# Kernel optimization log

Hardware: AMD Instinct MI355X
Metric: run time of the kernel (lower is better)

## Reference

```python
import jax, jax.numpy as jnp
import numpy as np

INPUT_DIM = 1024
NUM_HEADS = 16
HEAD_DIM = INPUT_DIM // NUM_HEADS


def setup_inputs() -> dict:
    key = jax.random.key(0)
    ks = jax.random.split(key, 9)
    d = INPUT_DIM
    s = 1.0 / np.sqrt(d)
    x = jax.random.normal(ks[0], (2, 2048, d), dtype=jnp.float32)
    # nn.Linear default init ~ U(-1/sqrt(in), 1/sqrt(in)); weights stored as (out, in), we keep (in, out)
    Wq = jax.random.uniform(ks[1], (d, d), jnp.float32, -s, s)
    bq = jax.random.uniform(ks[2], (d,), jnp.float32, -s, s)
    Wk = jax.random.uniform(ks[3], (d, d), jnp.float32, -s, s)
    bk = jax.random.uniform(ks[4], (d,), jnp.float32, -s, s)
    Wv = jax.random.uniform(ks[5], (d, d), jnp.float32, -s, s)
    bv = jax.random.uniform(ks[6], (d,), jnp.float32, -s, s)
    Wo = jax.random.uniform(ks[7], (d, d), jnp.float32, -s, s)
    bo = jax.random.uniform(ks[8], (d,), jnp.float32, -s, s)
    return {"x": x, "Wq": Wq, "bq": bq, "Wk": Wk, "bk": bk, "Wv": Wv, "bv": bv, "Wo": Wo, "bo": bo}


def reference(x, Wq, bq, Wk, bk, Wv, bv, Wo, bo):
    b, t, d = x.shape
    h, hd = NUM_HEADS, HEAD_DIM
    # projections -> [b, h, t, hd]
    q = (x @ Wq + bq).reshape(b, t, h, hd).transpose(0, 2, 1, 3)
    k = (x @ Wk + bk).reshape(b, t, h, hd).transpose(0, 2, 1, 3)
    v = (x @ Wv + bv).reshape(b, t, h, hd).transpose(0, 2, 1, 3)
    scores = jnp.einsum('bhqd,bhkd->bhqk', q, k) / jnp.sqrt(jnp.float32(hd))
    probs = jax.nn.softmax(scores, axis=-1)
    out = jnp.einsum('bhqk,bhkd->bhqd', probs, v)
    out = out.transpose(0, 2, 1, 3).reshape(b, t, d)
    return out @ Wo + bo
```

## Files before the change

### kernel.cpp

```cpp
#include <hip/hip_runtime.h>
#include <math.h>


#define BATCH 2
#define SEQ   2048
#define DIM   1024
#define NHEAD 16
#define HDIM  64
#define MROWS (BATCH * SEQ)
#define BH    (BATCH * NHEAD)
#define NKT   (SEQ / 64)

typedef __attribute__((ext_vector_type(4))) float     floatx4;
typedef __attribute__((ext_vector_type(4))) float     float4v;
typedef __attribute__((ext_vector_type(8))) _Float16  half8;
typedef __attribute__((ext_vector_type(4))) _Float16  half4;
typedef __attribute__((ext_vector_type(2))) __fp16    fp16x2;
typedef __attribute__((ext_vector_type(4))) unsigned  uint4v;

#define SOFT_C 5.77078016f
#define QSCALE 0.18033688f

#if __has_builtin(__builtin_amdgcn_exp2f)
#define EXP2F(x) __builtin_amdgcn_exp2f(x)
#else
#define EXP2F(x) exp2f(x)
#endif

__device__ __forceinline__ void gload16(const void* g, void* l) {
    __builtin_amdgcn_global_load_lds(
        (const __attribute__((address_space(1))) unsigned int*)g,
        (__attribute__((address_space(3))) unsigned int*)l, 16, 0, 0);
}

__device__ __forceinline__ unsigned pk2(float a, float b) {
    fp16x2 v = __builtin_amdgcn_cvt_pkrtz(a, b);
    return __builtin_bit_cast(unsigned, v);
}

__device__ __forceinline__ void plswap(unsigned &a, unsigned &b) {
#if __has_builtin(__builtin_amdgcn_permlane32_swap) && __has_builtin(__builtin_amdgcn_permlane16_swap)
    auto r32 = __builtin_amdgcn_permlane32_swap(a, b, false, false);
    auto r16 = __builtin_amdgcn_permlane16_swap(r32[0], r32[1], false, false);
    a = r16[0]; b = r16[1];
#else
    asm volatile("s_nop 1\n\t"
                 "v_permlane32_swap_b32 %0, %1\n\t"
                 "s_nop 1\n\t"
                 "v_permlane16_swap_b32 %0, %1\n\t"
                 "s_nop 1"
                 : "+v"(a), "+v"(b));
#endif
}

__global__ __launch_bounds__(256) void prep(
    const float* __restrict__ x,
    const float* __restrict__ Wq, const float* __restrict__ Wk,
    const float* __restrict__ Wv, const float* __restrict__ Wo,
    _Float16* __restrict__ xh,
    _Float16* __restrict__ Wqt, _Float16* __restrict__ Wkt,
    _Float16* __restrict__ Wvt, _Float16* __restrict__ Wot)
{
    const int tid = threadIdx.x;
    if (blockIdx.z == 4) {
        const int bid = blockIdx.y * 16 + blockIdx.x;
        #pragma unroll
        for (int it = 0; it < 8; ++it) {
            const size_t i = (((size_t)it * 256 + bid) * 256 + tid) * 8;
            float4v a = *(const float4v*)(x + i);
            float4v b = *(const float4v*)(x + i + 4);
            half8 o;
            #pragma unroll
            for (int c = 0; c < 4; ++c) { o[c] = (_Float16)a[c]; o[4+c] = (_Float16)b[c]; }
            *(half8*)(xh + i) = o;
        }
        return;
    }
    __shared__ float tile[64][65];
    const float* W; _Float16* o;
    switch (blockIdx.z) {
        case 0: W = Wq; o = Wqt; break;
        case 1: W = Wk; o = Wkt; break;
        case 2: W = Wv; o = Wvt; break;
        default: W = Wo; o = Wot; break;
    }
    const int n0 = blockIdx.x * 64, k0 = blockIdx.y * 64;
    #pragma unroll
    for (int p = 0; p < 16; ++p) {
        int idx = tid + p * 256;
        int r = idx >> 6, c = idx & 63;
        tile[r][c] = W[(size_t)(k0 + r) * DIM + n0 + c];
    }
    __syncthreads();
    #pragma unroll
    for (int p = 0; p < 16; ++p) {
        int idx = tid + p * 256;
        int r = idx >> 6, c = idx & 63;
        o[(size_t)(n0 + r) * DIM + k0 + c] = (_Float16)tile[c][r];
    }
}

__device__ __forceinline__ void gemm_core16(
    const _Float16* __restrict__ Ap, const _Float16* __restrict__ Bp,
    int m0, int n0, _Float16* AL, _Float16* BL, floatx4 acc[4][4])
{
    const int tid  = threadIdx.x;
    const int wave = tid >> 6;
    const int lane = tid & 63;
    const int li   = lane & 15;
    const int quad = lane >> 4;
    const int wm   = (wave >> 1) * 64;
    const int wn   = (wave & 1) * 64;

    for (int kt = 0; kt < DIM / 64; ++kt) {
        __syncthreads();
        const int k0 = kt * 64;
        #pragma unroll
        for (int p = 0; p < 4; ++p) {
            int s = tid + p * 256;
            int r = s >> 3, ks = s & 7;
            int kg = (ks ^ (r & 7)) << 3;
            int ldsb = (wave * 64 + p * 256) * 8;
            gload16(Ap + (size_t)(m0 + r) * DIM + k0 + kg, AL + ldsb);
            gload16(Bp + (size_t)(n0 + r) * DIM + k0 + kg, BL + ldsb);
        }
        __syncthreads();

        half8 a[4][2], b[4][2];
        #pragma unroll
        for (int i = 0; i < 4; ++i) {
            int ra = (wm + i * 16 + li) << 6;
            int rb = (wn + i * 16 + li) << 6;
            #pragma unroll
            for (int h = 0; h < 2; ++h) {
                a[i][h] = *(const half8*)(AL + ra + (((h * 4 + quad) ^ (li & 7)) << 3));
                b[i][h] = *(const half8*)(BL + rb + (((h * 4 + quad) ^ (li & 7)) << 3));
            }
        }
        #pragma unroll
        for (int i = 0; i < 4; ++i)
            #pragma unroll
            for (int j = 0; j < 4; ++j) {
                acc[i][j] = __builtin_amdgcn_mfma_f32_16x16x32_f16(a[i][0], b[j][0], acc[i][j], 0, 0, 0);
                acc[i][j] = __builtin_amdgcn_mfma_f32_16x16x32_f16(a[i][1], b[j][1], acc[i][j], 0, 0, 0);
            }
    }
}

__global__ __launch_bounds__(256, 2) void qkv_mfma(
    const _Float16* __restrict__ xh,
    const _Float16* __restrict__ Wqt, const _Float16* __restrict__ Wkt,
    const _Float16* __restrict__ Wvt,
    const float* __restrict__ bq, const float* __restrict__ bk,
    const float* __restrict__ bv,
    _Float16* __restrict__ Qh, _Float16* __restrict__ Kh,
    _Float16* __restrict__ Vth)
{
    __shared__ __align__(16) _Float16 SH[128 * 128];
    _Float16* AL = SH;
    _Float16* BL = SH + 128 * 64;

    const int bid = blockIdx.x + 8 * (blockIdx.y + 32 * blockIdx.z);
    const int swz = (bid & 7) * 96 + (bid >> 3);
    const int bx  = swz & 7;
    const int by  = (swz >> 3) & 31;
    const int z   = swz >> 8;

    const _Float16* Bp; const float* bias;
    if (z == 0)      { Bp = Wqt; bias = bq; }
    else if (z == 1) { Bp = Wkt; bias = bk; }
    else             { Bp = Wvt; bias = bv; }

    const int m0 = by * 128, n0 = bx * 128;

    floatx4 acc[4][4];
    #pragma unroll
    for (int i = 0; i < 4; ++i)
        #pragma unroll
        for (int j = 0; j < 4; ++j) acc[i][j] = (floatx4){0.f, 0.f, 0.f, 0.f};

    gemm_core16(xh, Bp, m0, n0, AL, BL, acc);

    const int tid = threadIdx.x, wave = tid >> 6, lane = tid & 63;
    const int li = lane & 15, quad = lane >> 4;
    const int wm = (wave >> 1) * 64, wn = (wave & 1) * 64;
    const int bb = m0 >> 11, t0 = m0 & 2047;

    if (z != 2) {
        _Float16* out = (z == 0) ? Qh : Kh;
        const float sc = (z == 0) ? QSCALE : 1.0f;
        #pragma unroll
        for (int i = 0; i < 4; ++i)
            #pragma unroll
            for (int j = 0; j < 4; ++j) {
                int n = n0 + wn + j * 16 + li;
                int h = n >> 6, hd = n & 63;
                float b_ = bias[n];
                #pragma unroll
                for (int r = 0; r < 4; ++r) {
                    int m = m0 + wm + i * 16 + quad * 4 + r;
                    int t = m & 2047;
                    out[(((size_t)(bb * NHEAD + h) * SEQ) + t) * HDIM + hd] =
                        (_Float16)((acc[i][j][r] + b_) * sc);
                }
            }
    } else {
        __syncthreads();
        #pragma unroll
        for (int i = 0; i < 4; ++i)
            #pragma unroll
            for (int j = 0; j < 4; ++j) {
                int n = wn + j * 16 + li;
                float b_ = bias[n0 + n];
                half4 w;
                #pragma unroll
                for (int r = 0; r < 4; ++r) w[r] = (_Float16)(acc[i][j][r] + b_);
                int col  = wm + i * 16 + quad * 4;
                int colp = ((((col >> 3) ^ (n & 7)) << 3)) | (col & 7);
                *(half4*)(SH + n * 128 + colp) = w;
            }
        __syncthreads();
        #pragma unroll
        for (int p = 0; p < 8; ++p) {
            int idx = p * 256 + tid;
            int v = idx >> 4, c8 = (idx & 15) * 8;
            int c8p = (((c8 >> 3) ^ (v & 7)) << 3);
            half8 w = *(const half8*)(SH + v * 128 + c8p);
            int n = n0 + v;
            int h = n >> 6, hd = n & 63;
            *(half8*)(Vth + ((size_t)(bb * NHEAD + h) * HDIM + hd) * SEQ + t0 + c8) = w;
        }
    }
}

__global__ __launch_bounds__(256, 4) void attn(
    const _Float16* __restrict__ Q, const _Float16* __restrict__ K,
    const _Float16* __restrict__ Vt,
    _Float16* __restrict__ Ctx)
{
    __shared__ __align__(16) _Float16 Ks[2][64 * 64];
    __shared__ __align__(16) _Float16 Vs[2][64 * 64];

    const int tid  = threadIdx.x;
    const int wave = tid >> 6;
    const int lane = tid & 63;
    const int li   = lane & 15;
    const int quad = lane >> 4;

    const int bid = blockIdx.x + 16 * blockIdx.y;
    const int swz = (bid & 7) * 64 + (bid >> 3);
    const int q0  = (swz & 15) * 128;
    const int bh  = swz >> 4;
    const int b   = bh >> 4, h = bh & 15;

    half8 qa[2][2];
    #pragma unroll
    for (int nq = 0; nq < 2; ++nq) {
        size_t qrow = ((size_t)bh * SEQ + q0 + wave * 32 + nq * 16 + li) * HDIM;
        qa[nq][0] = *(const half8*)(Q + qrow + quad * 8);
        qa[nq][1] = *(const half8*)(Q + qrow + 32 + quad * 8);
    }

    half8 onesA;
    {
        _Float16 v = (li == 0) ? (_Float16)1.0f : (_Float16)0.0f;
        #pragma unroll
        for (int c = 0; c < 8; ++c) onesA[c] = v;
    }

    floatx4 O[4][2];
    floatx4 rsacc[2];
    #pragma unroll
    for (int nq = 0; nq < 2; ++nq) {
        rsacc[nq] = (floatx4){0.f, 0.f, 0.f, 0.f};
        #pragma unroll
        for (int i = 0; i < 4; ++i) O[i][nq] = (floatx4){0.f, 0.f, 0.f, 0.f};
    }

    const _Float16* Kbh = K  + (size_t)bh * SEQ * HDIM;
    const _Float16* Vbh = Vt + (size_t)bh * HDIM * SEQ;

    auto stage = [&](int buf, int kt_) {
        const _Float16* Kg = Kbh + (size_t)kt_ * 64 * HDIM;
        const _Float16* Vg = Vbh + kt_ * 64;
        _Float16* Kl = &Ks[buf][0];
        _Float16* Vl = &Vs[buf][0];
        #pragma unroll
        for (int p = 0; p < 2; ++p) {
            int s = tid + p * 256;
            int r = s >> 3, ks = s & 7;
            int kg = (ks ^ (r & 7)) << 3;
            int ldsb = (wave * 64 + p * 256) * 8;
            gload16(Kg + r * HDIM + kg, Kl + ldsb);
            gload16(Vg + (size_t)r * SEQ + kg, Vl + ldsb);
        }
    };

    stage(0, 0);
    __syncthreads();
    int cur = 0;

    for (int kt = 0; kt < NKT; ++kt) {
        if (kt + 1 < NKT) stage(cur ^ 1, kt + 1);
        const _Float16* Kc = &Ks[cur][0];
        const _Float16* Vc = &Vs[cur][0];

        __builtin_amdgcn_s_setprio(1);

        unsigned R[2][4][2];
        #pragma unroll
        for (int mb = 0; mb < 4; ++mb) {
            int row = (mb * 16 + li) << 6;
            half8 a0 = *(const half8*)(Kc + row + ((quad ^ (li & 7)) << 3));
            half8 a1 = *(const half8*)(Kc + row + (((quad + 4) ^ (li & 7)) << 3));
            #pragma unroll
            for (int nq = 0; nq < 2; ++nq) {
                floatx4 st = (floatx4){-SOFT_C, -SOFT_C, -SOFT_C, -SOFT_C};
                st = __builtin_amdgcn_mfma_f32_16x16x32_f16(a0, qa[nq][0], st, 0, 0, 0);
                st = __builtin_amdgcn_mfma_f32_16x16x32_f16(a1, qa[nq][1], st, 0, 0, 0);
                R[nq][mb][0] = pk2(EXP2F(st[0]), EXP2F(st[1]));
                R[nq][mb][1] = pk2(EXP2F(st[2]), EXP2F(st[3]));
            }
        }

        half8 pb[2][2];
        #pragma unroll
        for (int nq = 0; nq < 2; ++nq)
            #pragma unroll
            for (int f = 0; f < 2; ++f) {
                unsigned w0, w1, w2, w3;
                {
                    unsigned x = R[nq][2 * f][0], y = R[nq][2 * f + 1][0];
                    plswap(x, y);
                    w0 = x; w2 = y;
                }
                {
                    unsigned x = R[nq][2 * f][1], y = R[nq][2 * f + 1][1];
                    plswap(x, y);
                    w1 = x; w3 = y;
                }
                uint4v uw; uw[0] = w0; uw[1] = w1; uw[2] = w2; uw[3] = w3;
                pb[nq][f] = __builtin_bit_cast(half8, uw);
            }

        #pragma unroll
        for (int nq = 0; nq < 2; ++nq) {
            rsacc[nq] = __builtin_amdgcn_mfma_f32_16x16x32_f16(onesA, pb[nq][0], rsacc[nq], 0, 0, 0);
            rsacc[nq] = __builtin_amdgcn_mfma_f32_16x16x32_f16(onesA, pb[nq][1], rsacc[nq], 0, 0, 0);
        }
        #pragma unroll
        for (int mb = 0; mb < 4; ++mb) {
            int row = (mb * 16 + li) << 6;
            half8 v0 = *(const half8*)(Vc + row + ((quad ^ (li & 7)) << 3));
            half8 v1 = *(const half8*)(Vc + row + (((quad + 4) ^ (li & 7)) << 3));
            #pragma unroll
            for (int nq = 0; nq < 2; ++nq) {
                O[mb][nq] = __builtin_amdgcn_mfma_f32_16x16x32_f16(v0, pb[nq][0], O[mb][nq], 0, 0, 0);
                O[mb][nq] = __builtin_amdgcn_mfma_f32_16x16x32_f16(v1, pb[nq][1], O[mb][nq], 0, 0, 0);
            }
        }

        __builtin_amdgcn_s_setprio(0);

        __syncthreads();
        cur ^= 1;
    }

    float inv[2];
    #pragma unroll
    for (int nq = 0; nq < 2; ++nq) {
        float rs = __shfl(rsacc[nq][0], li, 64);
        inv[nq] = 1.0f / rs;
    }

    _Float16* Sw = &Ks[0][0] + wave * (32 * 64);
    #pragma unroll
    for (int mb = 0; mb < 4; ++mb)
        #pragma unroll
        for (int nq = 0; nq < 2; ++nq) {
            uint2 w;
            w.x = pk2(O[mb][nq][0] * inv[nq], O[mb][nq][1] * inv[nq]);
            w.y = pk2(O[mb][nq][2] * inv[nq], O[mb][nq][3] * inv[nq]);
            int row = nq * 16 + li;
            int col = mb * 16 + quad * 4;
            int swc = (((col >> 3) ^ (row & 7)) << 3) | (col & 7);
            *(uint2*)(Sw + row * 64 + swc) = w;
        }
    __builtin_amdgcn_s_waitcnt(0);
    #pragma unroll
    for (int p = 0; p < 4; ++p) {
        int idx = p * 64 + lane;
        int qq = idx >> 3, c = idx & 7;
        half8 v = *(const half8*)(Sw + qq * 64 + ((c ^ (qq & 7)) << 3));
        size_t row = (size_t)b * SEQ + q0 + wave * 32 + qq;
        *(half8*)(Ctx + row * DIM + h * HDIM + c * 8) = v;
    }
}

__global__ __launch_bounds__(256, 2) void out_mfma(
    const _Float16* __restrict__ Ctx, const _Float16* __restrict__ Wot,
    const float* __restrict__ bo, float* __restrict__ out)
{
    __shared__ __align__(16) _Float16 AL[128 * 64];
    __shared__ __align__(16) _Float16 BL[128 * 64];

    const int bid = blockIdx.x + 8 * blockIdx.y;
    const int swz = (bid & 7) * 32 + (bid >> 3);
    const int m0 = (swz >> 3) * 128, n0 = (swz & 7) * 128;

    floatx4 acc[4][4];
    #pragma unroll
    for (int i = 0; i < 4; ++i)
        #pragma unroll
        for (int j = 0; j < 4; ++j) acc[i][j] = (floatx4){0.f, 0.f, 0.f, 0.f};

    gemm_core16(Ctx, Wot, m0, n0, AL, BL, acc);

    const int tid = threadIdx.x, wave = tid >> 6, lane = tid & 63;
    const int li = lane & 15, quad = lane >> 4;
    const int wm = (wave >> 1) * 64, wn = (wave & 1) * 64;

    #pragma unroll
    for (int i = 0; i < 4; ++i)
        #pragma unroll
        for (int j = 0; j < 4; ++j) {
            int n = n0 + wn + j * 16 + li;
            float b_ = bo[n];
            #pragma unroll
            for (int r = 0; r < 4; ++r) {
                int m = m0 + wm + i * 16 + quad * 4 + r;
                out[(size_t)m * DIM + n] = acc[i][j][r] + b_;
            }
        }
}

extern "C" void kernel_launch(void* const* d_in, const int* in_sizes, int n_in,
                              void* d_out, int out_size, void* d_ws, size_t ws_size,
                              hipStream_t stream) {
    const float* x  = (const float*)d_in[0];
    const float* Wq = (const float*)d_in[1];
    const float* bq = (const float*)d_in[2];
    const float* Wk = (const float*)d_in[3];
    const float* bk = (const float*)d_in[4];
    const float* Wv = (const float*)d_in[5];
    const float* bv = (const float*)d_in[6];
    const float* Wo = (const float*)d_in[7];
    const float* bo = (const float*)d_in[8];
    float* out = (float*)d_out;

    const size_t PX = (size_t)MROWS * DIM;
    const size_t PW = (size_t)DIM * DIM;
    _Float16* xh  = (_Float16*)d_ws;
    _Float16* Wqt = xh + PX;
    _Float16* Wkt = Wqt + PW;
    _Float16* Wvt = Wkt + PW;
    _Float16* Wot = Wvt + PW;
    _Float16* Qh  = Wot + PW;
    _Float16* Kh  = Qh + PX;
    _Float16* spare = Kh + PX;
    _Float16* Vth = spare + PX;

    _Float16* Ctx = xh;

    prep<<<dim3(16, 16, 5), 256, 0, stream>>>(
        x, Wq, Wk, Wv, Wo, xh, Wqt, Wkt, Wvt, Wot);

    qkv_mfma<<<dim3(DIM / 128, MROWS / 128, 3), 256, 0, stream>>>(
        xh, Wqt, Wkt, Wvt, bq, bk, bv, Qh, Kh, Vth);

    attn<<<dim3(SEQ / 128, BH), 256, 0, stream>>>(
        Qh, Kh, Vth, Ctx);

    out_mfma<<<dim3(DIM / 128, MROWS / 128), 256, 0, stream>>>(
        Ctx, Wot, bo, out);
}
```

Measured before the change: 179.7 us.

## Split attention head dimension of V across two blocks to double grid size

```diff
diff --git a/kernel.cpp b/kernel.cpp
--- a/kernel.cpp
+++ b/kernel.cpp
@@ -239,7 +239,7 @@
     _Float16* __restrict__ Ctx)
 {
     __shared__ __align__(16) _Float16 Ks[2][64 * 64];
-    __shared__ __align__(16) _Float16 Vs[2][64 * 64];
+    __shared__ __align__(16) _Float16 Vs[2][32 * 64];
 
     const int tid  = threadIdx.x;
     const int wave = tid >> 6;
@@ -247,11 +247,13 @@
     const int li   = lane & 15;
     const int quad = lane >> 4;
 
-    const int bid = blockIdx.x + 16 * blockIdx.y;
-    const int swz = (bid & 7) * 64 + (bid >> 3);
+    const int bid = blockIdx.x + 16 * (blockIdx.y + 2 * blockIdx.z);
+    const int swz = (bid & 7) * 128 + (bid >> 3);
     const int q0  = (swz & 15) * 128;
-    const int bh  = swz >> 4;
+    const int hh  = (swz >> 4) & 1;
+    const int bh  = swz >> 5;
     const int b   = bh >> 4, h = bh & 15;
+    const int hd0 = hh * 32;
 
     half8 qa[2][2];
     #pragma unroll
@@ -268,17 +270,17 @@
         for (int c = 0; c < 8; ++c) onesA[c] = v;
     }
 
-    floatx4 O[4][2];
+    floatx4 O[2][2];
     floatx4 rsacc[2];
     #pragma unroll
     for (int nq = 0; nq < 2; ++nq) {
         rsacc[nq] = (floatx4){0.f, 0.f, 0.f, 0.f};
         #pragma unroll
-        for (int i = 0; i < 4; ++i) O[i][nq] = (floatx4){0.f, 0.f, 0.f, 0.f};
+        for (int i = 0; i < 2; ++i) O[i][nq] = (floatx4){0.f, 0.f, 0.f, 0.f};
     }
 
     const _Float16* Kbh = K  + (size_t)bh * SEQ * HDIM;
-    const _Float16* Vbh = Vt + (size_t)bh * HDIM * SEQ;
+    const _Float16* Vbh = Vt + ((size_t)bh * HDIM + hd0) * SEQ;
 
     auto stage = [&](int buf, int kt_) {
         const _Float16* Kg = Kbh + (size_t)kt_ * 64 * HDIM;
@@ -290,9 +292,12 @@
             int s = tid + p * 256;
             int r = s >> 3, ks = s & 7;
             int kg = (ks ^ (r & 7)) << 3;
-            int ldsb = (wave * 64 + p * 256) * 8;
-            gload16(Kg + r * HDIM + kg, Kl + ldsb);
-            gload16(Vg + (size_t)r * SEQ + kg, Vl + ldsb);
+            gload16(Kg + r * HDIM + kg, Kl + (wave * 64 + p * 256) * 8);
+        }
+        {
+            int r = tid >> 3, ks = tid & 7;
+            int kg = (ks ^ (r & 7)) << 3;
+            gload16(Vg + (size_t)r * SEQ + kg, Vl + wave * 64 * 8);
         }
     };
 
@@ -349,14 +354,14 @@
             rsacc[nq] = __builtin_amdgcn_mfma_f32_16x16x32_f16(onesA, pb[nq][1], rsacc[nq], 0, 0, 0);
         }
         #pragma unroll
-        for (int mb = 0; mb < 4; ++mb) {
-            int row = (mb * 16 + li) << 6;
+        for (int vb = 0; vb < 2; ++vb) {
+            int row = (vb * 16 + li) << 6;
             half8 v0 = *(const half8*)(Vc + row + ((quad ^ (li & 7)) << 3));
             half8 v1 = *(const half8*)(Vc + row + (((quad + 4) ^ (li & 7)) << 3));
             #pragma unroll
             for (int nq = 0; nq < 2; ++nq) {
-                O[mb][nq] = __builtin_amdgcn_mfma_f32_16x16x32_f16(v0, pb[nq][0], O[mb][nq], 0, 0, 0);
-                O[mb][nq] = __builtin_amdgcn_mfma_f32_16x16x32_f16(v1, pb[nq][1], O[mb][nq], 0, 0, 0);
+                O[vb][nq] = __builtin_amdgcn_mfma_f32_16x16x32_f16(v0, pb[nq][0], O[vb][nq], 0, 0, 0);
+                O[vb][nq] = __builtin_amdgcn_mfma_f32_16x16x32_f16(v1, pb[nq][1], O[vb][nq], 0, 0, 0);
             }
         }
 
@@ -373,27 +378,27 @@
         inv[nq] = 1.0f / rs;
     }
 
-    _Float16* Sw = &Ks[0][0] + wave * (32 * 64);
-    #pragma unroll
-    for (int mb = 0; mb < 4; ++mb)
+    _Float16* Sw = &Ks[0][0] + wave * (32 * 32);
+    #pragma unroll
+    for (int vb = 0; vb < 2; ++vb)
         #pragma unroll
         for (int nq = 0; nq < 2; ++nq) {
             uint2 w;
-            w.x = pk2(O[mb][nq][0] * inv[nq], O[mb][nq][1] * inv[nq]);
-            w.y = pk2(O[mb][nq][2] * inv[nq], O[mb][nq][3] * inv[nq]);
+            w.x = pk2(O[vb][nq][0] * inv[nq], O[vb][nq][1] * inv[nq]);
+            w.y = pk2(O[vb][nq][2] * inv[nq], O[vb][nq][3] * inv[nq]);
             int row = nq * 16 + li;
-            int col = mb * 16 + quad * 4;
-            int swc = (((col >> 3) ^ (row & 7)) << 3) | (col & 7);
-            *(uint2*)(Sw + row * 64 + swc) = w;
+            int col = vb * 16 + quad * 4;
+            int swc = (((col >> 3) ^ (row & 3)) << 3) | (col & 7);
+            *(uint2*)(Sw + row * 32 + swc) = w;
         }
     __builtin_amdgcn_s_waitcnt(0);
     #pragma unroll
-    for (int p = 0; p < 4; ++p) {
+    for (int p = 0; p < 2; ++p) {
         int idx = p * 64 + lane;
-        int qq = idx >> 3, c = idx & 7;
-        half8 v = *(const half8*)(Sw + qq * 64 + ((c ^ (qq & 7)) << 3));
+        int qq = idx >> 2, c = idx & 3;
+        half8 v = *(const half8*)(Sw + qq * 32 + ((c ^ (qq & 3)) << 3));
         size_t row = (size_t)b * SEQ + q0 + wave * 32 + qq;
-        *(half8*)(Ctx + row * DIM + h * HDIM + c * 8) = v;
+        *(half8*)(Ctx + row * DIM + h * HDIM + hd0 + c * 8) = v;
     }
 }
 
@@ -468,7 +473,7 @@
     qkv_mfma<<<dim3(DIM / 128, MROWS / 128, 3), 256, 0, stream>>>(
         xh, Wqt, Wkt, Wvt, bq, bk, bv, Qh, Kh, Vth);
 
-    attn<<<dim3(SEQ / 128, BH), 256, 0, stream>>>(
+    attn<<<dim3(SEQ / 128, 2, BH), 256, 0, stream>>>(
         Qh, Kh, Vth, Ctx);
 
     out_mfma<<<dim3(DIM / 128, MROWS / 128), 256, 0, stream>>>(
```

After: 196.8 us. 9.5% more time.

## Software-pipeline attention loop so PV of previous tile overlaps QK of next

Applied to the files above, without the earlier changes.

```diff
diff --git a/kernel.cpp b/kernel.cpp
--- a/kernel.cpp
+++ b/kernel.cpp
@@ -233,7 +233,7 @@
     }
 }
 
-__global__ __launch_bounds__(256, 4) void attn(
+__global__ __launch_bounds__(256, 2) void attn(
     const _Float16* __restrict__ Q, const _Float16* __restrict__ K,
     const _Float16* __restrict__ Vt,
     _Float16* __restrict__ Ctx)
@@ -296,17 +296,8 @@
         }
     };
 
-    stage(0, 0);
-    __syncthreads();
-    int cur = 0;
-
-    for (int kt = 0; kt < NKT; ++kt) {
-        if (kt + 1 < NKT) stage(cur ^ 1, kt + 1);
-        const _Float16* Kc = &Ks[cur][0];
-        const _Float16* Vc = &Vs[cur][0];
-
-        __builtin_amdgcn_s_setprio(1);
-
+    auto qk_phase = [&](const _Float16* Kc, const _Float16* Vc,
+                        half8 (&pbN)[2][2], half8 (&vfN)[4][2]) {
         unsigned R[2][4][2];
         #pragma unroll
         for (int mb = 0; mb < 4; ++mb) {
@@ -322,8 +313,6 @@
                 R[nq][mb][1] = pk2(EXP2F(st[2]), EXP2F(st[3]));
             }
         }
-
-        half8 pb[2][2];
         #pragma unroll
         for (int nq = 0; nq < 2; ++nq)
             #pragma unroll
@@ -340,31 +329,65 @@
                     w1 = x; w3 = y;
                 }
                 uint4v uw; uw[0] = w0; uw[1] = w1; uw[2] = w2; uw[3] = w3;
-                pb[nq][f] = __builtin_bit_cast(half8, uw);
-            }
-
-        #pragma unroll
-        for (int nq = 0; nq < 2; ++nq) {
-            rsacc[nq] = __builtin_amdgcn_mfma_f32_16x16x32_f16(onesA, pb[nq][0], rsacc[nq], 0, 0, 0);
-            rsacc[nq] = __builtin_amdgcn_mfma_f32_16x16x32_f16(onesA, pb[nq][1], rsacc[nq], 0, 0, 0);
-        }
+                pbN[nq][f] = __builtin_bit_cast(half8, uw);
+            }
         #pragma unroll
         for (int mb = 0; mb < 4; ++mb) {
             int row = (mb * 16 + li) << 6;
-            half8 v0 = *(const half8*)(Vc + row + ((quad ^ (li & 7)) << 3));
-            half8 v1 = *(const half8*)(Vc + row + (((quad + 4) ^ (li & 7)) << 3));
+            vfN[mb][0] = *(const half8*)(Vc + row + ((quad ^ (li & 7)) << 3));
+            vfN[mb][1] = *(const half8*)(Vc + row + (((quad + 4) ^ (li & 7)) << 3));
+        }
+    };
+
+    auto pv_phase = [&](half8 (&pbP)[2][2], half8 (&vfP)[4][2]) {
+        #pragma unroll
+        for (int nq = 0; nq < 2; ++nq) {
+            rsacc[nq] = __builtin_amdgcn_mfma_f32_16x16x32_f16(onesA, pbP[nq][0], rsacc[nq], 0, 0, 0);
+            rsacc[nq] = __builtin_amdgcn_mfma_f32_16x16x32_f16(onesA, pbP[nq][1], rsacc[nq], 0, 0, 0);
+        }
+        #pragma unroll
+        for (int mb = 0; mb < 4; ++mb)
             #pragma unroll
             for (int nq = 0; nq < 2; ++nq) {
-                O[mb][nq] = __builtin_amdgcn_mfma_f32_16x16x32_f16(v0, pb[nq][0], O[mb][nq], 0, 0, 0);
-                O[mb][nq] = __builtin_amdgcn_mfma_f32_16x16x32_f16(v1, pb[nq][1], O[mb][nq], 0, 0, 0);
-            }
-        }
-
+                O[mb][nq] = __builtin_amdgcn_mfma_f32_16x16x32_f16(vfP[mb][0], pbP[nq][0], O[mb][nq], 0, 0, 0);
+                O[mb][nq] = __builtin_amdgcn_mfma_f32_16x16x32_f16(vfP[mb][1], pbP[nq][1], O[mb][nq], 0, 0, 0);
+            }
+    };
+
+    half8 pbA[2][2], pbB[2][2];
+    half8 vfA[4][2], vfB[4][2];
+
+    stage(0, 0);
+    __syncthreads();
+
+    stage(1, 1);
+    __builtin_amdgcn_s_setprio(1);
+    qk_phase(&Ks[0][0], &Vs[0][0], pbA, vfA);
+    __builtin_amdgcn_s_setprio(0);
+    __syncthreads();
+
+    for (int kt = 1; kt < NKT - 1; kt += 2) {
+        stage(0, kt + 1);
+        __builtin_amdgcn_s_setprio(1);
+        pv_phase(pbA, vfA);
+        qk_phase(&Ks[1][0], &Vs[1][0], pbB, vfB);
         __builtin_amdgcn_s_setprio(0);
-
-        __syncthreads();
-        cur ^= 1;
-    }
+        __syncthreads();
+
+        stage(1, kt + 2);
+        __builtin_amdgcn_s_setprio(1);
+        pv_phase(pbB, vfB);
+        qk_phase(&Ks[0][0], &Vs[0][0], pbA, vfA);
+        __builtin_amdgcn_s_setprio(0);
+        __syncthreads();
+    }
+
+    __builtin_amdgcn_s_setprio(1);
+    pv_phase(pbA, vfA);
+    qk_phase(&Ks[1][0], &Vs[1][0], pbB, vfB);
+    pv_phase(pbB, vfB);
+    __builtin_amdgcn_s_setprio(0);
+    __syncthreads();
 
     float inv[2];
     #pragma unroll
```

After: 177.7 us. Within noise of the previous version (-1.2%).
